# Optimization experiments

Hardware: AMD Instinct MI355X
Metric: run time of the kernel (lower is better)

Reference implementation:

```python
import jax, jax.numpy as jnp
import numpy as np

DIM = 1024
HEADS = 16
HEAD_DIM = DIM // HEADS
B, T = 2, 2048


def setup_inputs() -> dict:
    key = jax.random.key(0)
    ks = jax.random.split(key, 6)
    x = jax.random.normal(ks[0], (B, T, DIM), dtype=jnp.float32)
    # Linear weights stored as [in, out] for x @ W + b
    w_qkv = jax.random.normal(ks[1], (DIM, 3 * DIM), dtype=jnp.float32) * (1.0 / np.sqrt(DIM))
    b_qkv = jnp.zeros((3 * DIM,), dtype=jnp.float32)
    w_out = jax.random.normal(ks[2], (DIM, DIM), dtype=jnp.float32) * (1.0 / np.sqrt(DIM))
    b_out = jnp.zeros((DIM,), dtype=jnp.float32)
    pos_bias = jax.random.normal(ks[3], (1, HEADS, 1, HEAD_DIM), dtype=jnp.float32) * 0.1
    return {"x": x, "w_qkv": w_qkv, "b_qkv": b_qkv, "w_out": w_out, "b_out": b_out, "pos_bias": pos_bias}


def reference(x, w_qkv, b_qkv, w_out, b_out, pos_bias):
    b, t, c = x.shape
    scale = HEAD_DIM ** -0.5
    qkv = x @ w_qkv + b_qkv                       # [B, T, 3C]
    q, k, v = jnp.split(qkv, 3, axis=-1)
    # [B, T, C] -> [B, H, T, Dh]
    def to_heads(z):
        return z.reshape(b, t, HEADS, HEAD_DIM).transpose(0, 2, 1, 3)
    q = to_heads(q) + pos_bias                    # learned query positional bias
    k = to_heads(k)
    v = to_heads(v)
    attn = jnp.einsum('bhqd,bhkd->bhqk', q, k) * scale
    causal = jnp.tril(jnp.ones((t, t), dtype=bool))
    attn = jnp.where(causal[None, None], attn, -jnp.inf)
    attn = jax.nn.softmax(attn, axis=-1)
    out = jnp.einsum('bhqk,bhkd->bhqd', attn, v)  # [B, H, T, Dh]
    out = out.transpose(0, 2, 1, 3).reshape(b, t, c)
    # dropout inactive (eval mode)
    return out @ w_out + b_out
```

## Files before the change

kernel.cpp:

```cpp
#include <hip/hip_runtime.h>

#define DIM 1024
#define HEADS 16
#define HD 64
#define BATCH 2
#define SEQ 2048
#define MROWS (BATCH*SEQ)
#define NQKV (3*DIM)
#define BK 32
#define NT (DIM/BK)
#define ALDT 72

typedef unsigned short u16;
typedef __attribute__((ext_vector_type(8))) short short8;
typedef __attribute__((ext_vector_type(4))) float f32x4;

#define QSCALE 0.1803368801111204f
#define DTHR 11.5f

__device__ __forceinline__ u16 f2bf(float f) {
  unsigned u = __float_as_uint(f);
  u += 0x7FFFu + ((u >> 16) & 1u);
  return (u16)(u >> 16);
}

__device__ __forceinline__ unsigned cvtpk(float lo, float hi) {
  unsigned r;
  asm("v_cvt_pk_bf16_f32 %0, %1, %2" : "=v"(r) : "v"(lo), "v"(hi));
  return r;
}

__device__ __forceinline__ void gload16(const u16* g, u16* l) {
  __builtin_amdgcn_global_load_lds((const __attribute__((address_space(1))) unsigned int*)g,
                                   (__attribute__((address_space(3))) unsigned int*)l, 16, 0, 0);
}

__global__ void k_f32_to_bf16(const float* __restrict__ in, u16* __restrict__ out, int n8) {
  int i = blockIdx.x * blockDim.x + threadIdx.x;
  if (i >= n8) return;
  const float4* p = (const float4*)in + (size_t)i * 2;
  float4 a = p[0], b = p[1];
  short8 v;
  v[0] = (short)f2bf(a.x); v[1] = (short)f2bf(a.y);
  v[2] = (short)f2bf(a.z); v[3] = (short)f2bf(a.w);
  v[4] = (short)f2bf(b.x); v[5] = (short)f2bf(b.y);
  v[6] = (short)f2bf(b.z); v[7] = (short)f2bf(b.w);
  ((short8*)out)[i] = v;
}

__global__ void k_transpose2(const float* __restrict__ wqkv, u16* __restrict__ oqkv,
                             const float* __restrict__ wout, u16* __restrict__ oout) {
  __shared__ float tile[32][33];
  const int bx = blockIdx.x;
  const float* in; u16* out; int C, c0;
  if (bx < 96) { in = wqkv; out = oqkv; C = NQKV; c0 = bx * 32; }
  else         { in = wout; out = oout; C = DIM;  c0 = (bx - 96) * 32; }
  const int r0 = blockIdx.y * 32;
  const int tx = threadIdx.x, ty = threadIdx.y;
#pragma unroll
  for (int i = 0; i < 4; ++i)
    tile[ty + 8 * i][tx] = in[(size_t)(r0 + ty + 8 * i) * C + c0 + tx];
  __syncthreads();
#pragma unroll
  for (int i = 0; i < 4; ++i)
    out[(size_t)(c0 + ty + 8 * i) * DIM + r0 + tx] = f2bf(tile[tx][ty + 8 * i]);
}

#define GEMM_PREAMBLE(Aptr, Bptr)                                              \
  __shared__ u16 lds_[4 * 8192];                                               \
  const int tid = threadIdx.x;                                                 \
  const int lane = tid & 63;                                                   \
  const int wid = tid >> 6;                                                    \
  const int wm = wid >> 1, wn = wid & 1;                                       \
  const int rowA0 = blockIdx.y * 128;                                          \
  const int rowB0 = blockIdx.x * 128;                                          \
  const int rl = lane & 15, lg = lane >> 4;                                    \
  const int csw = (rl >> 1) & 3;                                               \
  const f32x4 fz = {0.f, 0.f, 0.f, 0.f};                                       \
  f32x4 acc[4][4];                                                             \
  _Pragma("unroll") for (int i = 0; i < 4; ++i)                                \
  _Pragma("unroll") for (int j = 0; j < 4; ++j) acc[i][j] = fz;                \
  const int srow = tid >> 2;                                                   \
  const int scol = ((tid & 3) ^ ((tid >> 3) & 3)) * 8;                         \
  const u16* gA = (Aptr) + (size_t)(rowA0 + srow) * DIM + scol;                \
  const u16* gB = (Bptr) + (size_t)(rowB0 + srow) * DIM + scol;                \
  auto stage = [&](int t, int j) {                                             \
    u16* d = lds_ + j * 8192;                                                  \
    gload16(gA + t * BK, d + tid * 8);                                         \
    gload16(gA + (size_t)64 * DIM + t * BK, d + 2048 + tid * 8);               \
    gload16(gB + t * BK, d + 4096 + tid * 8);                                  \
    gload16(gB + (size_t)64 * DIM + t * BK, d + 6144 + tid * 8);               \
  };                                                                           \
  auto compute = [&](int j) {                                                  \
    const u16* bufA = lds_ + j * 8192;                                         \
    const u16* bufB = bufA + 4096;                                             \
    short8 af[4], bfr[4];                                                      \
    _Pragma("unroll") for (int mf = 0; mf < 4; ++mf)                           \
      af[mf] = *(const short8*)(bufA + (wm * 64 + mf * 16 + rl) * 32 +         \
                                ((lg ^ csw) * 8));                             \
    _Pragma("unroll") for (int nf = 0; nf < 4; ++nf)                           \
      bfr[nf] = *(const short8*)(bufB + (wn * 64 + nf * 16 + rl) * 32 +        \
                                 ((lg ^ csw) * 8));                            \
    __builtin_amdgcn_s_setprio(1);                                             \
    _Pragma("unroll") for (int mf = 0; mf < 4; ++mf)                           \
    _Pragma("unroll") for (int nf = 0; nf < 4; ++nf)                           \
      acc[mf][nf] =                                                            \
          __builtin_amdgcn_mfma_f32_16x16x32_bf16(af[mf], bfr[nf],             \
                                                  acc[mf][nf], 0, 0, 0);       \
    __builtin_amdgcn_s_setprio(0);                                             \
  };                                                                           \
  stage(0, 0);                                                                 \
  stage(1, 1);                                                                 \
  stage(2, 2);                                                                 \
  asm volatile("s_waitcnt vmcnt(8)" ::: "memory");                             \
  __builtin_amdgcn_s_barrier();                                                \
  _Pragma("unroll 4") for (int t = 0; t < NT; ++t) {                           \
    if (t + 3 < NT) {                                                          \
      stage(t + 3, (t + 3) & 3);                                               \
      compute(t & 3);                                                          \
      asm volatile("s_waitcnt vmcnt(8)" ::: "memory");                         \
      __builtin_amdgcn_s_barrier();                                            \
    } else if (t == NT - 3) {                                                  \
      compute(t & 3);                                                          \
      asm volatile("s_waitcnt vmcnt(4)" ::: "memory");                         \
      __builtin_amdgcn_s_barrier();                                            \
    } else if (t == NT - 2) {                                                  \
      compute(t & 3);                                                          \
      asm volatile("s_waitcnt vmcnt(0)" ::: "memory");                         \
      __builtin_amdgcn_s_barrier();                                            \
    } else {                                                                   \
      compute(t & 3);                                                          \
    }                                                                          \
  }

__global__ __launch_bounds__(256) void k_gemm_qkv(
    const u16* __restrict__ A, const u16* __restrict__ Bt,
    const float* __restrict__ bias, const float* __restrict__ posb,
    u16* __restrict__ qb, u16* __restrict__ kb, u16* __restrict__ vtb) {
  GEMM_PREAMBLE(A, Bt)

#pragma unroll
  for (int mf = 0; mf < 4; ++mf) {
#pragma unroll
    for (int nf = 0; nf < 4; ++nf) {
#pragma unroll
      for (int r = 0; r < 4; ++r) {
        const int row = rowA0 + wm * 64 + mf * 16 + lg * 4 + r;
        const int col = rowB0 + wn * 64 + nf * 16 + rl;
        float v = acc[mf][nf][r] + bias[col];
        const int which = col >> 10;
        const int within = col & 1023;
        const int h = within >> 6, d = within & 63;
        const int bb = row >> 11, t = row & 2047;
        const size_t bh = (size_t)(bb * HEADS + h);
        if (which == 0) {
          v = (v + posb[within]) * QSCALE;
          qb[(bh * SEQ + t) * HD + d] = f2bf(v);
        } else if (which == 1) {
          kb[(bh * SEQ + t) * HD + d] = f2bf(v);
        } else {
          vtb[(bh * HD + d) * SEQ + t] = f2bf(v);
        }
      }
    }
  }
}

__global__ __launch_bounds__(256) void k_gemm_out(
    const u16* __restrict__ A, const u16* __restrict__ Bt,
    const float* __restrict__ bias, float* __restrict__ out) {
  __shared__ u16 lds_[4 * 6144];
  const int tid = threadIdx.x;
  const int lane = tid & 63;
  const int wid = tid >> 6;
  const int wm = wid >> 1, wn = wid & 1;
  const int rowA0 = blockIdx.y * 128;
  const int rowB0 = blockIdx.x * 64;
  const int rl = lane & 15, lg = lane >> 4;
  const int csw = (rl >> 1) & 3;
  const f32x4 fz = {0.f, 0.f, 0.f, 0.f};
  f32x4 acc[4][2];
#pragma unroll
  for (int i = 0; i < 4; ++i)
#pragma unroll
    for (int j = 0; j < 2; ++j) acc[i][j] = fz;
  const int srow = tid >> 2;
  const int scol = ((tid & 3) ^ ((tid >> 3) & 3)) * 8;
  const u16* gA = A + (size_t)(rowA0 + srow) * DIM + scol;
  const u16* gB = Bt + (size_t)(rowB0 + srow) * DIM + scol;
  auto stage = [&](int t, int j) {
    u16* d = lds_ + j * 6144;
    gload16(gA + t * BK, d + tid * 8);
    gload16(gA + (size_t)64 * DIM + t * BK, d + 2048 + tid * 8);
    gload16(gB + t * BK, d + 4096 + tid * 8);
  };
  auto compute = [&](int j) {
    const u16* bufA = lds_ + j * 6144;
    const u16* bufB = bufA + 4096;
    short8 af[4], bfr[2];
#pragma unroll
    for (int mf = 0; mf < 4; ++mf)
      af[mf] = *(const short8*)(bufA + (wm * 64 + mf * 16 + rl) * 32 + ((lg ^ csw) * 8));
#pragma unroll
    for (int nf = 0; nf < 2; ++nf)
      bfr[nf] = *(const short8*)(bufB + (wn * 32 + nf * 16 + rl) * 32 + ((lg ^ csw) * 8));
    __builtin_amdgcn_s_setprio(1);
#pragma unroll
    for (int mf = 0; mf < 4; ++mf)
#pragma unroll
      for (int nf = 0; nf < 2; ++nf)
        acc[mf][nf] = __builtin_amdgcn_mfma_f32_16x16x32_bf16(af[mf], bfr[nf], acc[mf][nf], 0, 0, 0);
    __builtin_amdgcn_s_setprio(0);
  };
  stage(0, 0);
  stage(1, 1);
  stage(2, 2);
  asm volatile("s_waitcnt vmcnt(6)" ::: "memory");
  __builtin_amdgcn_s_barrier();
#pragma unroll 4
  for (int t = 0; t < NT; ++t) {
    if (t + 3 < NT) {
      stage(t + 3, (t + 3) & 3);
      compute(t & 3);
      asm volatile("s_waitcnt vmcnt(6)" ::: "memory");
      __builtin_amdgcn_s_barrier();
    } else if (t == NT - 3) {
      compute(t & 3);
      asm volatile("s_waitcnt vmcnt(3)" ::: "memory");
      __builtin_amdgcn_s_barrier();
    } else if (t == NT - 2) {
      compute(t & 3);
      asm volatile("s_waitcnt vmcnt(0)" ::: "memory");
      __builtin_amdgcn_s_barrier();
    } else {
      compute(t & 3);
    }
  }

#pragma unroll
  for (int mf = 0; mf < 4; ++mf)
#pragma unroll
    for (int nf = 0; nf < 2; ++nf)
#pragma unroll
      for (int r = 0; r < 4; ++r) {
        const int row = rowA0 + wm * 64 + mf * 16 + lg * 4 + r;
        const int col = rowB0 + wn * 32 + nf * 16 + rl;
        out[(size_t)row * DIM + col] = acc[mf][nf][r] + bias[col];
      }
}

__global__ __launch_bounds__(256) void k_attn(
    const u16* __restrict__ qg, const u16* __restrict__ kg, const u16* __restrict__ vg,
    u16* __restrict__ og) {
  __shared__ u16 lK[2][64 * ALDT];
  __shared__ u16 lV[2][64 * ALDT];
  __shared__ u16 lP[4 * 16 * ALDT];
  const int tid = threadIdx.x;
  const int lane = tid & 63;
  const int wid = tid >> 6;
  const int rl = lane & 15, lg = lane >> 4;
  const int bh = blockIdx.x & 31;
  const int pair = blockIdx.x >> 5;
  const int b = bh >> 4, h = bh & 15;

  const u16* gK = kg + (size_t)bh * SEQ * HD;
  const u16* gV = vg + (size_t)bh * HD * SEQ;
  const int sr = tid >> 3;
  const int sc = (tid & 7) * 8;
  u16* pw = lP + wid * 16 * ALDT;

#pragma unroll 1
  for (int half = 0; half < 2; ++half) {
    const int qt = half ? pair : (31 - pair);
    const int qrow = qt * 64 + wid * 16 + rl;
    const u16* qptr = qg + ((size_t)bh * SEQ + qrow) * HD + lg * 8;
    const short8 aq0 = *(const short8*)(qptr);
    const short8 aq1 = *(const short8*)(qptr + 32);

    const f32x4 fz = {0.f, 0.f, 0.f, 0.f};
    f32x4 o[4];
#pragma unroll
    for (int dt = 0; dt < 4; ++dt) o[dt] = fz;
    float m = -1e30f, l = 0.f;

    int4 rka = *(const int4*)(gK + (size_t)sr * HD + sc);
    int4 rkb = *(const int4*)(gK + (size_t)(sr + 32) * HD + sc);
    int4 rva = *(const int4*)(gV + (size_t)sr * SEQ + sc);
    int4 rvb = *(const int4*)(gV + (size_t)(sr + 32) * SEQ + sc);
    *(int4*)(lK[0] + sr * ALDT + sc) = rka;
    *(int4*)(lK[0] + (sr + 32) * ALDT + sc) = rkb;
    *(int4*)(lV[0] + sr * ALDT + sc) = rva;
    *(int4*)(lV[0] + (sr + 32) * ALDT + sc) = rvb;
    if (qt > 0) {
      rka = *(const int4*)(gK + (size_t)(64 + sr) * HD + sc);
      rkb = *(const int4*)(gK + (size_t)(64 + sr + 32) * HD + sc);
      rva = *(const int4*)(gV + (size_t)sr * SEQ + 64 + sc);
      rvb = *(const int4*)(gV + (size_t)(sr + 32) * SEQ + 64 + sc);
    }
    asm volatile("s_waitcnt lgkmcnt(0)" ::: "memory");
    __builtin_amdgcn_s_barrier();

    for (int kt = 0; kt <= qt; ++kt) {
      const int cur = kt & 1;
      if (kt < qt) {
        u16* dK = lK[cur ^ 1];
        u16* dV = lV[cur ^ 1];
        *(int4*)(dK + sr * ALDT + sc) = rka;
        *(int4*)(dK + (sr + 32) * ALDT + sc) = rkb;
        *(int4*)(dV + sr * ALDT + sc) = rva;
        *(int4*)(dV + (sr + 32) * ALDT + sc) = rvb;
        if (kt + 2 <= qt) {
          const int kv2 = (kt + 2) * 64;
          rka = *(const int4*)(gK + (size_t)(kv2 + sr) * HD + sc);
          rkb = *(const int4*)(gK + (size_t)(kv2 + sr + 32) * HD + sc);
          rva = *(const int4*)(gV + (size_t)sr * SEQ + kv2 + sc);
          rvb = *(const int4*)(gV + (size_t)(sr + 32) * SEQ + kv2 + sc);
        }
      }
      const u16* bK = lK[cur];
      const u16* bV = lV[cur];

      f32x4 s[4];
#pragma unroll
      for (int ct = 0; ct < 4; ++ct) s[ct] = fz;
      __builtin_amdgcn_s_setprio(1);
#pragma unroll
      for (int ct = 0; ct < 4; ++ct) {
        short8 ak0 = *(const short8*)(bK + (ct * 16 + rl) * ALDT + lg * 8);
        short8 ak1 = *(const short8*)(bK + (ct * 16 + rl) * ALDT + 32 + lg * 8);
        s[ct] = __builtin_amdgcn_mfma_f32_16x16x32_bf16(ak0, aq0, s[ct], 0, 0, 0);
        s[ct] = __builtin_amdgcn_mfma_f32_16x16x32_bf16(ak1, aq1, s[ct], 0, 0, 0);
      }
      __builtin_amdgcn_s_setprio(0);

      if (kt == qt) {
#pragma unroll
        for (int ct = 0; ct < 4; ++ct)
#pragma unroll
          for (int r = 0; r < 4; ++r)
            if (kt * 64 + ct * 16 + lg * 4 + r > qrow) s[ct][r] = -1e30f;
      }

      float cm[4];
#pragma unroll
      for (int ct = 0; ct < 4; ++ct)
        cm[ct] = fmaxf(fmaxf(s[ct][0], s[ct][1]), fmaxf(s[ct][2], s[ct][3]));
      float pmax = fmaxf(fmaxf(cm[0], cm[1]), fmaxf(cm[2], cm[3]));
      pmax = fmaxf(pmax, __shfl_xor(pmax, 16, 64));
      pmax = fmaxf(pmax, __shfl_xor(pmax, 32, 64));

      if (__any(pmax - m > DTHR)) {
        const float mn = fmaxf(m, pmax);
        const float alpha = __builtin_amdgcn_exp2f(m - mn);
        m = mn;
        l *= alpha;
#pragma unroll
        for (int dt = 0; dt < 4; ++dt)
#pragma unroll
          for (int r = 0; r < 4; ++r) o[dt][r] *= alpha;
      }

      float rc[4];
#pragma unroll
      for (int ct = 0; ct < 4; ++ct) {
        float p0 = __builtin_amdgcn_exp2f(s[ct][0] - m);
        float p1 = __builtin_amdgcn_exp2f(s[ct][1] - m);
        float p2 = __builtin_amdgcn_exp2f(s[ct][2] - m);
        float p3 = __builtin_amdgcn_exp2f(s[ct][3] - m);
        rc[ct] = (p0 + p1) + (p2 + p3);
        uint2 w;
        w.x = cvtpk(p0, p1);
        w.y = cvtpk(p2, p3);
        *(uint2*)(pw + rl * ALDT + ct * 16 + lg * 4) = w;
      }
      l += (rc[0] + rc[1]) + (rc[2] + rc[3]);

#pragma unroll
      for (int kb2 = 0; kb2 < 2; ++kb2) {
        short8 pa = *(const short8*)(pw + rl * ALDT + kb2 * 32 + lg * 8);
        __builtin_amdgcn_s_setprio(1);
#pragma unroll
        for (int dt = 0; dt < 4; ++dt) {
          short8 av = *(const short8*)(bV + (dt * 16 + rl) * ALDT + kb2 * 32 + lg * 8);
          o[dt] = __builtin_amdgcn_mfma_f32_16x16x32_bf16(av, pa, o[dt], 0, 0, 0);
        }
        __builtin_amdgcn_s_setprio(0);
      }

      asm volatile("s_waitcnt lgkmcnt(0)" ::: "memory");
      __builtin_amdgcn_s_barrier();
    }

    l += __shfl_xor(l, 16, 64);
    l += __shfl_xor(l, 32, 64);
    const float linv = __builtin_amdgcn_rcpf(l);
    const size_t obase = ((size_t)b * SEQ + qrow) * DIM + h * HD;
#pragma unroll
    for (int dt = 0; dt < 4; ++dt) {
      uint2 w;
      w.x = cvtpk(o[dt][0] * linv, o[dt][1] * linv);
      w.y = cvtpk(o[dt][2] * linv, o[dt][3] * linv);
      *(uint2*)(og + obase + dt * 16 + lg * 4) = w;
    }
  }
}

extern "C" void kernel_launch(void* const* d_in, const int* in_sizes, int n_in,
                              void* d_out, int out_size, void* d_ws, size_t ws_size,
                              hipStream_t stream) {
  const float* x = (const float*)d_in[0];
  const float* w_qkv = (const float*)d_in[1];
  const float* b_qkv = (const float*)d_in[2];
  const float* w_out = (const float*)d_in[3];
  const float* b_out = (const float*)d_in[4];
  const float* pos_bias = (const float*)d_in[5];
  float* out = (float*)d_out;

  u16* ws = (u16*)d_ws;
  u16* xb = ws;
  u16* wqkvb = xb + (size_t)MROWS * DIM;
  u16* woutb = wqkvb + (size_t)NQKV * DIM;
  u16* qb = woutb + (size_t)DIM * DIM;
  u16* kbuf = qb + (size_t)BATCH * HEADS * SEQ * HD;
  u16* vtb = kbuf + (size_t)BATCH * HEADS * SEQ * HD;
  u16* attnb = xb;

  k_f32_to_bf16<<<(MROWS * DIM / 8 + 255) / 256, 256, 0, stream>>>(x, xb, MROWS * DIM / 8);
  k_transpose2<<<dim3(128, DIM / 32), dim3(32, 8), 0, stream>>>(w_qkv, wqkvb, w_out, woutb);
  k_gemm_qkv<<<dim3(NQKV / 128, MROWS / 128), 256, 0, stream>>>(xb, wqkvb, b_qkv, pos_bias, qb, kbuf, vtb);
  k_attn<<<dim3(BATCH * HEADS * 16), 256, 0, stream>>>(qb, kbuf, vtb, attnb);
  k_gemm_out<<<dim3(DIM / 64, MROWS / 128), 256, 0, stream>>>(attnb, woutb, b_out, out);
}
```

Measured before the change: 194.8 us.

## Fuse prep kernels, remap GEMM blocks across XCDs, widen attention KV tiles

Merges the fp32-to-bf16 conversion and the two weight transposes into one launch, and remaps GEMM block indices so that neighbouring tiles are spread across the eight XCDs for better L2 locality. The attention kernel now processes 128-key tiles per iteration. It also redistributes the softmax probabilities for the PV MFMA through lane shuffles instead of writing and reading them through LDS. The aim is fewer launches, fewer barriers per key, and no LDS round trip for P, at the cost of more registers and a causal tile granularity coarser than the 64-row query tiles.

```diff
diff --git a/kernel.cpp b/kernel.cpp
--- a/kernel.cpp
+++ b/kernel.cpp
@@ -9,7 +9,8 @@
 #define NQKV (3*DIM)
 #define BK 32
 #define NT (DIM/BK)
-#define ALDT 72
+#define KLDT 72
+#define VLDT 136
 
 typedef unsigned short u16;
 typedef __attribute__((ext_vector_type(8))) short short8;
@@ -35,28 +36,36 @@
                                    (__attribute__((address_space(3))) unsigned int*)l, 16, 0, 0);
 }
 
-__global__ void k_f32_to_bf16(const float* __restrict__ in, u16* __restrict__ out, int n8) {
-  int i = blockIdx.x * blockDim.x + threadIdx.x;
-  if (i >= n8) return;
-  const float4* p = (const float4*)in + (size_t)i * 2;
-  float4 a = p[0], b = p[1];
-  short8 v;
-  v[0] = (short)f2bf(a.x); v[1] = (short)f2bf(a.y);
-  v[2] = (short)f2bf(a.z); v[3] = (short)f2bf(a.w);
-  v[4] = (short)f2bf(b.x); v[5] = (short)f2bf(b.y);
-  v[6] = (short)f2bf(b.z); v[7] = (short)f2bf(b.w);
-  ((short8*)out)[i] = v;
-}
-
-__global__ void k_transpose2(const float* __restrict__ wqkv, u16* __restrict__ oqkv,
-                             const float* __restrict__ wout, u16* __restrict__ oout) {
+__global__ __launch_bounds__(256) void k_prep(
+    const float* __restrict__ x, u16* __restrict__ xb,
+    const float* __restrict__ wqkv, u16* __restrict__ oqkv,
+    const float* __restrict__ wout, u16* __restrict__ oout) {
   __shared__ float tile[32][33];
-  const int bx = blockIdx.x;
-  const float* in; u16* out; int C, c0;
-  if (bx < 96) { in = wqkv; out = oqkv; C = NQKV; c0 = bx * 32; }
-  else         { in = wout; out = oout; C = DIM;  c0 = (bx - 96) * 32; }
-  const int r0 = blockIdx.y * 32;
-  const int tx = threadIdx.x, ty = threadIdx.y;
+  const int bid = blockIdx.x;
+  const int tid = threadIdx.x;
+  if (bid < 2048) {
+    const int i = bid * 256 + tid;
+    const float4* p = (const float4*)x + (size_t)i * 2;
+    float4 a = p[0], b = p[1];
+    short8 v;
+    v[0] = (short)f2bf(a.x); v[1] = (short)f2bf(a.y);
+    v[2] = (short)f2bf(a.z); v[3] = (short)f2bf(a.w);
+    v[4] = (short)f2bf(b.x); v[5] = (short)f2bf(b.y);
+    v[6] = (short)f2bf(b.z); v[7] = (short)f2bf(b.w);
+    ((short8*)xb)[i] = v;
+    return;
+  }
+  const float* in; u16* out; int C, c0, r0;
+  if (bid < 2048 + 3072) {
+    const int idx = bid - 2048;
+    in = wqkv; out = oqkv; C = NQKV;
+    c0 = (idx % 96) * 32; r0 = (idx / 96) * 32;
+  } else {
+    const int idx = bid - 5120;
+    in = wout; out = oout; C = DIM;
+    c0 = (idx & 31) * 32; r0 = (idx >> 5) * 32;
+  }
+  const int tx = tid & 31, ty = tid >> 5;
 #pragma unroll
   for (int i = 0; i < 4; ++i)
     tile[ty + 8 * i][tx] = in[(size_t)(r0 + ty + 8 * i) * C + c0 + tx];
@@ -66,14 +75,16 @@
     out[(size_t)(c0 + ty + 8 * i) * DIM + r0 + tx] = f2bf(tile[tx][ty + 8 * i]);
 }
 
-#define GEMM_PREAMBLE(Aptr, Bptr)                                              \
+#define GEMM_PREAMBLE(Aptr, Bptr, GX, NWGS)                                    \
   __shared__ u16 lds_[4 * 8192];                                               \
   const int tid = threadIdx.x;                                                 \
   const int lane = tid & 63;                                                   \
   const int wid = tid >> 6;                                                    \
   const int wm = wid >> 1, wn = wid & 1;                                       \
-  const int rowA0 = blockIdx.y * 128;                                          \
-  const int rowB0 = blockIdx.x * 128;                                          \
+  const int bid_ = blockIdx.x;                                                 \
+  const int wg_ = (bid_ & 7) * ((NWGS) / 8) + (bid_ >> 3);                     \
+  const int rowB0 = (wg_ % (GX)) * 128;                                        \
+  const int rowA0 = (wg_ / (GX)) * 128;                                        \
   const int rl = lane & 15, lg = lane >> 4;                                    \
   const int csw = (rl >> 1) & 3;                                               \
   const f32x4 fz = {0.f, 0.f, 0.f, 0.f};                                       \
@@ -137,7 +148,7 @@
     const u16* __restrict__ A, const u16* __restrict__ Bt,
     const float* __restrict__ bias, const float* __restrict__ posb,
     u16* __restrict__ qb, u16* __restrict__ kb, u16* __restrict__ vtb) {
-  GEMM_PREAMBLE(A, Bt)
+  GEMM_PREAMBLE(A, Bt, 24, 768)
 
 #pragma unroll
   for (int mf = 0; mf < 4; ++mf) {
@@ -174,8 +185,10 @@
   const int lane = tid & 63;
   const int wid = tid >> 6;
   const int wm = wid >> 1, wn = wid & 1;
-  const int rowA0 = blockIdx.y * 128;
-  const int rowB0 = blockIdx.x * 64;
+  const int bid_ = blockIdx.x;
+  const int wg_ = (bid_ & 7) * 64 + (bid_ >> 3);
+  const int rowB0 = (wg_ & 15) * 64;
+  const int rowA0 = (wg_ >> 4) * 128;
   const int rl = lane & 15, lg = lane >> 4;
   const int csw = (rl >> 1) & 3;
   const f32x4 fz = {0.f, 0.f, 0.f, 0.f};
@@ -252,9 +265,8 @@
 __global__ __launch_bounds__(256) void k_attn(
     const u16* __restrict__ qg, const u16* __restrict__ kg, const u16* __restrict__ vg,
     u16* __restrict__ og) {
-  __shared__ u16 lK[2][64 * ALDT];
-  __shared__ u16 lV[2][64 * ALDT];
-  __shared__ u16 lP[4 * 16 * ALDT];
+  __shared__ u16 lK[2][128 * KLDT];
+  __shared__ u16 lV[2][64 * VLDT];
   const int tid = threadIdx.x;
   const int lane = tid & 63;
   const int wid = tid >> 6;
@@ -267,11 +279,14 @@
   const u16* gV = vg + (size_t)bh * HD * SEQ;
   const int sr = tid >> 3;
   const int sc = (tid & 7) * 8;
-  u16* pw = lP + wid * 16 * ALDT;
+  const int sl0 = (((2 * lg) & 3) << 4) + rl;
+  const int sl1 = (((2 * lg + 1) & 3) << 4) + rl;
+  const bool hi = (lg >= 2);
 
 #pragma unroll 1
   for (int half = 0; half < 2; ++half) {
     const int qt = half ? pair : (31 - pair);
+    const int nt = (qt >> 1) + 1;
     const int qrow = qt * 64 + wid * 16 + rl;
     const u16* qptr = qg + ((size_t)bh * SEQ + qrow) * HD + lg * 8;
     const short8 aq0 = *(const short8*)(qptr);
@@ -283,69 +298,89 @@
     for (int dt = 0; dt < 4; ++dt) o[dt] = fz;
     float m = -1e30f, l = 0.f;
 
-    int4 rka = *(const int4*)(gK + (size_t)sr * HD + sc);
-    int4 rkb = *(const int4*)(gK + (size_t)(sr + 32) * HD + sc);
-    int4 rva = *(const int4*)(gV + (size_t)sr * SEQ + sc);
-    int4 rvb = *(const int4*)(gV + (size_t)(sr + 32) * SEQ + sc);
-    *(int4*)(lK[0] + sr * ALDT + sc) = rka;
-    *(int4*)(lK[0] + (sr + 32) * ALDT + sc) = rkb;
-    *(int4*)(lV[0] + sr * ALDT + sc) = rva;
-    *(int4*)(lV[0] + (sr + 32) * ALDT + sc) = rvb;
-    if (qt > 0) {
-      rka = *(const int4*)(gK + (size_t)(64 + sr) * HD + sc);
-      rkb = *(const int4*)(gK + (size_t)(64 + sr + 32) * HD + sc);
-      rva = *(const int4*)(gV + (size_t)sr * SEQ + 64 + sc);
-      rvb = *(const int4*)(gV + (size_t)(sr + 32) * SEQ + 64 + sc);
+    int4 rk[4], rv[4];
+#pragma unroll
+    for (int i = 0; i < 4; ++i) {
+      rk[i] = *(const int4*)(gK + (size_t)(i * 32 + sr) * HD + sc);
+      rv[i & 1] = rv[i & 1];
+    }
+    rv[0] = *(const int4*)(gV + (size_t)sr * SEQ + sc);
+    rv[1] = *(const int4*)(gV + (size_t)sr * SEQ + 64 + sc);
+    rv[2] = *(const int4*)(gV + (size_t)(sr + 32) * SEQ + sc);
+    rv[3] = *(const int4*)(gV + (size_t)(sr + 32) * SEQ + 64 + sc);
+#pragma unroll
+    for (int i = 0; i < 4; ++i)
+      *(int4*)(lK[0] + (i * 32 + sr) * KLDT + sc) = rk[i];
+    *(int4*)(lV[0] + sr * VLDT + sc) = rv[0];
+    *(int4*)(lV[0] + sr * VLDT + 64 + sc) = rv[1];
+    *(int4*)(lV[0] + (sr + 32) * VLDT + sc) = rv[2];
+    *(int4*)(lV[0] + (sr + 32) * VLDT + 64 + sc) = rv[3];
+    if (nt > 1) {
+#pragma unroll
+      for (int i = 0; i < 4; ++i)
+        rk[i] = *(const int4*)(gK + (size_t)(128 + i * 32 + sr) * HD + sc);
+      rv[0] = *(const int4*)(gV + (size_t)sr * SEQ + 128 + sc);
+      rv[1] = *(const int4*)(gV + (size_t)sr * SEQ + 192 + sc);
+      rv[2] = *(const int4*)(gV + (size_t)(sr + 32) * SEQ + 128 + sc);
+      rv[3] = *(const int4*)(gV + (size_t)(sr + 32) * SEQ + 192 + sc);
     }
     asm volatile("s_waitcnt lgkmcnt(0)" ::: "memory");
     __builtin_amdgcn_s_barrier();
 
-    for (int kt = 0; kt <= qt; ++kt) {
+    for (int kt = 0; kt < nt; ++kt) {
       const int cur = kt & 1;
-      if (kt < qt) {
+      if (kt + 1 < nt) {
         u16* dK = lK[cur ^ 1];
         u16* dV = lV[cur ^ 1];
-        *(int4*)(dK + sr * ALDT + sc) = rka;
-        *(int4*)(dK + (sr + 32) * ALDT + sc) = rkb;
-        *(int4*)(dV + sr * ALDT + sc) = rva;
-        *(int4*)(dV + (sr + 32) * ALDT + sc) = rvb;
-        if (kt + 2 <= qt) {
-          const int kv2 = (kt + 2) * 64;
-          rka = *(const int4*)(gK + (size_t)(kv2 + sr) * HD + sc);
-          rkb = *(const int4*)(gK + (size_t)(kv2 + sr + 32) * HD + sc);
-          rva = *(const int4*)(gV + (size_t)sr * SEQ + kv2 + sc);
-          rvb = *(const int4*)(gV + (size_t)(sr + 32) * SEQ + kv2 + sc);
+#pragma unroll
+        for (int i = 0; i < 4; ++i)
+          *(int4*)(dK + (i * 32 + sr) * KLDT + sc) = rk[i];
+        *(int4*)(dV + sr * VLDT + sc) = rv[0];
+        *(int4*)(dV + sr * VLDT + 64 + sc) = rv[1];
+        *(int4*)(dV + (sr + 32) * VLDT + sc) = rv[2];
+        *(int4*)(dV + (sr + 32) * VLDT + 64 + sc) = rv[3];
+        if (kt + 2 < nt) {
+          const int kv2 = (kt + 2) * 128;
+#pragma unroll
+          for (int i = 0; i < 4; ++i)
+            rk[i] = *(const int4*)(gK + (size_t)(kv2 + i * 32 + sr) * HD + sc);
+          rv[0] = *(const int4*)(gV + (size_t)sr * SEQ + kv2 + sc);
+          rv[1] = *(const int4*)(gV + (size_t)sr * SEQ + kv2 + 64 + sc);
+          rv[2] = *(const int4*)(gV + (size_t)(sr + 32) * SEQ + kv2 + sc);
+          rv[3] = *(const int4*)(gV + (size_t)(sr + 32) * SEQ + kv2 + 64 + sc);
         }
       }
       const u16* bK = lK[cur];
       const u16* bV = lV[cur];
-
-      f32x4 s[4];
-#pragma unroll
-      for (int ct = 0; ct < 4; ++ct) s[ct] = fz;
+      const int kv0 = kt * 128;
+
+      f32x4 s[8];
+#pragma unroll
+      for (int ct = 0; ct < 8; ++ct) s[ct] = fz;
       __builtin_amdgcn_s_setprio(1);
 #pragma unroll
-      for (int ct = 0; ct < 4; ++ct) {
-        short8 ak0 = *(const short8*)(bK + (ct * 16 + rl) * ALDT + lg * 8);
-        short8 ak1 = *(const short8*)(bK + (ct * 16 + rl) * ALDT + 32 + lg * 8);
+      for (int ct = 0; ct < 8; ++ct) {
+        short8 ak0 = *(const short8*)(bK + (ct * 16 + rl) * KLDT + lg * 8);
+        short8 ak1 = *(const short8*)(bK + (ct * 16 + rl) * KLDT + 32 + lg * 8);
         s[ct] = __builtin_amdgcn_mfma_f32_16x16x32_bf16(ak0, aq0, s[ct], 0, 0, 0);
         s[ct] = __builtin_amdgcn_mfma_f32_16x16x32_bf16(ak1, aq1, s[ct], 0, 0, 0);
       }
       __builtin_amdgcn_s_setprio(0);
 
-      if (kt == qt) {
-#pragma unroll
-        for (int ct = 0; ct < 4; ++ct)
+      if (kt == nt - 1) {
+#pragma unroll
+        for (int ct = 0; ct < 8; ++ct)
 #pragma unroll
           for (int r = 0; r < 4; ++r)
-            if (kt * 64 + ct * 16 + lg * 4 + r > qrow) s[ct][r] = -1e30f;
-      }
-
-      float cm[4];
-#pragma unroll
-      for (int ct = 0; ct < 4; ++ct)
+            if (kv0 + ct * 16 + lg * 4 + r > qrow) s[ct][r] = -1e30f;
+      }
+
+      float cm[8];
+#pragma unroll
+      for (int ct = 0; ct < 8; ++ct)
         cm[ct] = fmaxf(fmaxf(s[ct][0], s[ct][1]), fmaxf(s[ct][2], s[ct][3]));
-      float pmax = fmaxf(fmaxf(cm[0], cm[1]), fmaxf(cm[2], cm[3]));
+      float pmax = fmaxf(fmaxf(fmaxf(cm[0], cm[1]), fmaxf(cm[2], cm[3])),
+                         fmaxf(fmaxf(cm[4], cm[5]), fmaxf(cm[6], cm[7])));
       pmax = fmaxf(pmax, __shfl_xor(pmax, 16, 64));
       pmax = fmaxf(pmax, __shfl_xor(pmax, 32, 64));
 
@@ -360,29 +395,40 @@
           for (int r = 0; r < 4; ++r) o[dt][r] *= alpha;
       }
 
-      float rc[4];
-#pragma unroll
-      for (int ct = 0; ct < 4; ++ct) {
+      float rc[8];
+      unsigned pk[8][2];
+#pragma unroll
+      for (int ct = 0; ct < 8; ++ct) {
         float p0 = __builtin_amdgcn_exp2f(s[ct][0] - m);
         float p1 = __builtin_amdgcn_exp2f(s[ct][1] - m);
         float p2 = __builtin_amdgcn_exp2f(s[ct][2] - m);
         float p3 = __builtin_amdgcn_exp2f(s[ct][3] - m);
         rc[ct] = (p0 + p1) + (p2 + p3);
-        uint2 w;
-        w.x = cvtpk(p0, p1);
-        w.y = cvtpk(p2, p3);
-        *(uint2*)(pw + rl * ALDT + ct * 16 + lg * 4) = w;
-      }
-      l += (rc[0] + rc[1]) + (rc[2] + rc[3]);
-
-#pragma unroll
-      for (int kb2 = 0; kb2 < 2; ++kb2) {
-        short8 pa = *(const short8*)(pw + rl * ALDT + kb2 * 32 + lg * 8);
+        pk[ct][0] = cvtpk(p0, p1);
+        pk[ct][1] = cvtpk(p2, p3);
+      }
+      l += ((rc[0] + rc[1]) + (rc[2] + rc[3])) + ((rc[4] + rc[5]) + (rc[6] + rc[7]));
+
+#pragma unroll
+      for (int kb2 = 0; kb2 < 4; ++kb2) {
+        unsigned a0 = (unsigned)__shfl((int)pk[2 * kb2 + 0][0], sl0, 64);
+        unsigned b0 = (unsigned)__shfl((int)pk[2 * kb2 + 1][0], sl0, 64);
+        unsigned a1 = (unsigned)__shfl((int)pk[2 * kb2 + 0][1], sl0, 64);
+        unsigned b1 = (unsigned)__shfl((int)pk[2 * kb2 + 1][1], sl0, 64);
+        unsigned a2 = (unsigned)__shfl((int)pk[2 * kb2 + 0][0], sl1, 64);
+        unsigned b2 = (unsigned)__shfl((int)pk[2 * kb2 + 1][0], sl1, 64);
+        unsigned a3 = (unsigned)__shfl((int)pk[2 * kb2 + 0][1], sl1, 64);
+        unsigned b3 = (unsigned)__shfl((int)pk[2 * kb2 + 1][1], sl1, 64);
+        union { unsigned u[4]; short8 s8; } pu;
+        pu.u[0] = hi ? b0 : a0;
+        pu.u[1] = hi ? b1 : a1;
+        pu.u[2] = hi ? b2 : a2;
+        pu.u[3] = hi ? b3 : a3;
         __builtin_amdgcn_s_setprio(1);
 #pragma unroll
         for (int dt = 0; dt < 4; ++dt) {
-          short8 av = *(const short8*)(bV + (dt * 16 + rl) * ALDT + kb2 * 32 + lg * 8);
-          o[dt] = __builtin_amdgcn_mfma_f32_16x16x32_bf16(av, pa, o[dt], 0, 0, 0);
+          short8 av = *(const short8*)(bV + (dt * 16 + rl) * VLDT + kb2 * 32 + lg * 8);
+          o[dt] = __builtin_amdgcn_mfma_f32_16x16x32_bf16(av, pu.s8, o[dt], 0, 0, 0);
         }
         __builtin_amdgcn_s_setprio(0);
       }
@@ -425,9 +471,8 @@
   u16* vtb = kbuf + (size_t)BATCH * HEADS * SEQ * HD;
   u16* attnb = xb;
 
-  k_f32_to_bf16<<<(MROWS * DIM / 8 + 255) / 256, 256, 0, stream>>>(x, xb, MROWS * DIM / 8);
-  k_transpose2<<<dim3(128, DIM / 32), dim3(32, 8), 0, stream>>>(w_qkv, wqkvb, w_out, woutb);
-  k_gemm_qkv<<<dim3(NQKV / 128, MROWS / 128), 256, 0, stream>>>(xb, wqkvb, b_qkv, pos_bias, qb, kbuf, vtb);
+  k_prep<<<6144, 256, 0, stream>>>(x, xb, w_qkv, wqkvb, w_out, woutb);
+  k_gemm_qkv<<<768, 256, 0, stream>>>(xb, wqkvb, b_qkv, pos_bias, qb, kbuf, vtb);
   k_attn<<<dim3(BATCH * HEADS * 16), 256, 0, stream>>>(qb, kbuf, vtb, attnb);
-  k_gemm_out<<<dim3(DIM / 64, MROWS / 128), 256, 0, stream>>>(attnb, woutb, b_out, out);
-}
+  k_gemm_out<<<512, 256, 0, stream>>>(attnb, woutb, b_out, out);
+}
```

Measured after the change: 241.8 us. 1.24x slower.
